# Performance work log

Measured on AMD Instinct MI355X. Metric: run time of the kernel, lower is better.

The kernel has to match this reference:

```python
import jax, jax.numpy as jnp
import numpy as np

B, D, KM1 = 8192, 256, 64  # batch, feature dim (no bias), num_classes-1
NC = KM1 + 1


def setup_inputs() -> dict:
    key = jax.random.key(0)
    k1, k2, k3 = jax.random.split(key, 3)
    features = jax.random.normal(k1, (B, D), dtype=jnp.float32)
    y = jax.random.randint(k2, (B,), 0, NC)
    mu = jax.random.normal(k3, (D, KM1), dtype=jnp.float32) * 0.001
    Sigma = jnp.broadcast_to(jnp.eye(D, dtype=jnp.float32), (KM1, D, D)).copy()
    return {"features": features, "y": y, "mu": mu, "Sigma": Sigma, "loss_type": 1}


def _b_ky(nc):
    # (nc, nc-1) stick-breaking selector matrix
    return 1.0 - jnp.pad(jnp.eye(nc)[..., :-2], [(0, 0), (1, 0)]).cumsum(-1)


def reference(features, y, mu, Sigma, loss_type):
    x = features                      # use_bias=False -> pad is a no-op
    logits = x @ mu                   # (B, K-1)
    bky = _b_ky(NC)                   # (K, K-1)
    y1h = jax.nn.one_hot(y, NC)       # (B, K)
    if loss_type == 0:
        full = jnp.pad(logits, [(0, 0), (0, 1)]) - jax.nn.softplus(logits) @ bky.T
        return -jnp.sum(full * y1h, -1)
    else:
        # psi_k = sqrt(x^T (Sigma_k + mu_k mu_k^T) x) = sqrt(x^T Sigma_k x + (x.mu_k)^2)
        xSx = jnp.einsum('bd,kde,be->bk', x, Sigma, x)   # (B, K-1)
        psi = jnp.sqrt(xSx + logits * logits)
        b = y1h @ bky                 # (B, K-1)
        kappa = y1h[..., :-1] - b / 2
        return -jnp.sum(logits * kappa + b * (psi / 2 - jax.nn.softplus(psi)), -1)
```

## Files before the change

### kernel.cpp

```cpp
#include <hip/hip_runtime.h>

typedef __attribute__((ext_vector_type(8))) short bf16x8;
typedef __attribute__((ext_vector_type(4))) float f32x4;

#define B_N 8192
#define D_N 256
#define K_N 64

__device__ __forceinline__ unsigned short bf16_rne(float f) {
  unsigned u = __builtin_bit_cast(unsigned, f);
  u += 0x7fffu + ((u >> 16) & 1u);
  return (unsigned short)(u >> 16);
}
__device__ __forceinline__ float bf16_f32(unsigned short h) {
  return __builtin_bit_cast(float, (unsigned)h << 16);
}

__device__ __forceinline__ void gload_lds16(const void* g, void* l) {
  __builtin_amdgcn_global_load_lds(
      (const __attribute__((address_space(1))) unsigned int*)g,
      (__attribute__((address_space(3))) unsigned int*)l, 16, 0, 0);
}

__global__ void convert_kernel(const float* __restrict__ src,
                               ushort* __restrict__ hi, ushort* __restrict__ lo,
                               int n4) {
  int idx = blockIdx.x * blockDim.x + threadIdx.x;
  int stride = gridDim.x * blockDim.x;
  for (int i = idx; i < n4; i += stride) {
    float4 v = ((const float4*)src)[i];
    ushort4 h, l;
    h.x = bf16_rne(v.x); l.x = bf16_rne(v.x - bf16_f32(h.x));
    h.y = bf16_rne(v.y); l.y = bf16_rne(v.y - bf16_f32(h.y));
    h.z = bf16_rne(v.z); l.z = bf16_rne(v.z - bf16_f32(h.z));
    h.w = bf16_rne(v.w); l.w = bf16_rne(v.w - bf16_f32(h.w));
    ((ushort4*)hi)[i] = h;
    ((ushort4*)lo)[i] = l;
  }
}

__global__ __launch_bounds__(256, 3) void xsx64_kernel(
    const float* __restrict__ X,
    const ushort* __restrict__ Xh, const ushort* __restrict__ Xl,
    const ushort* __restrict__ Sh, const ushort* __restrict__ Sl,
    float* __restrict__ xsx) {
  __shared__ __align__(16) ushort smem[20480];
  ushort(*Ah)[32] = (ushort(*)[32])(smem);
  ushort(*Al)[32] = (ushort(*)[32])(smem + 2048);
  ushort(*Bh)[32] = (ushort(*)[32])(smem + 4096);
  ushort(*Bl)[32] = (ushort(*)[32])(smem + 12288);
  float(*red)[64] = (float(*)[64])(smem);

  const int tid = threadIdx.x;
  const int lane = tid & 63;
  const int wid = tid >> 6;
  const int lr = lane & 15;
  const int lk = lane >> 4;

  const int bid = blockIdx.x;
  const int xcd = bid & 7;
  const int j = bid >> 3;
  const int kk = xcd * 8 + (j & 7);
  const int b0 = (j >> 3) * 64;
  const size_t soff = (size_t)kk * D_N * D_N;

  const int srow = lane >> 2;
  const int sc = ((lane & 3) ^ ((lane >> 3) & 3)) * 8;
  const int rdc = (lk ^ ((lr >> 1) & 3)) * 8;

  f32x4 acc[4][4];
#pragma unroll
  for (int mi = 0; mi < 4; ++mi)
#pragma unroll
    for (int ni = 0; ni < 4; ++ni) acc[mi][ni] = (f32x4){0.f, 0.f, 0.f, 0.f};

  const size_t arow = (size_t)(b0 + wid * 16 + srow) * D_N + sc;

  for (int ec = 0; ec < 8; ++ec) {
    const int e0 = ec * 32;
    __syncthreads();
    gload_lds16(Xh + arow + e0, &Ah[wid * 16][0]);
    gload_lds16(Xl + arow + e0, &Al[wid * 16][0]);
#pragma unroll
    for (int i = 0; i < 4; ++i) {
      const size_t brow =
          soff + (size_t)(wid * 64 + i * 16 + srow) * D_N + sc + e0;
      gload_lds16(Sh + brow, &Bh[wid * 64 + i * 16][0]);
      gload_lds16(Sl + brow, &Bl[wid * 64 + i * 16][0]);
    }
    __syncthreads();

    bf16x8 ah[4], al[4];
#pragma unroll
    for (int mi = 0; mi < 4; ++mi) {
      ah[mi] = *(const bf16x8*)&Ah[mi * 16 + lr][rdc];
      al[mi] = *(const bf16x8*)&Al[mi * 16 + lr][rdc];
    }
#pragma unroll
    for (int ni = 0; ni < 4; ++ni) {
      const bf16x8 bh = *(const bf16x8*)&Bh[wid * 64 + ni * 16 + lr][rdc];
      const bf16x8 bl = *(const bf16x8*)&Bl[wid * 64 + ni * 16 + lr][rdc];
#pragma unroll
      for (int mi = 0; mi < 4; ++mi)
        acc[mi][ni] = __builtin_amdgcn_mfma_f32_16x16x32_bf16(
            ah[mi], bh, acc[mi][ni], 0, 0, 0);
#pragma unroll
      for (int mi = 0; mi < 4; ++mi)
        acc[mi][ni] = __builtin_amdgcn_mfma_f32_16x16x32_bf16(
            al[mi], bh, acc[mi][ni], 0, 0, 0);
#pragma unroll
      for (int mi = 0; mi < 4; ++mi)
        acc[mi][ni] = __builtin_amdgcn_mfma_f32_16x16x32_bf16(
            ah[mi], bl, acc[mi][ni], 0, 0, 0);
    }
  }

  float p[4][4];
#pragma unroll
  for (int mi = 0; mi < 4; ++mi)
#pragma unroll
    for (int jj = 0; jj < 4; ++jj) p[mi][jj] = 0.f;
#pragma unroll
  for (int mi = 0; mi < 4; ++mi) {
#pragma unroll
    for (int jj = 0; jj < 4; ++jj) {
      const int brow = b0 + mi * 16 + lk * 4 + jj;
      const float* xr = X + (size_t)brow * D_N + wid * 64 + lr;
#pragma unroll
      for (int ni = 0; ni < 4; ++ni)
        p[mi][jj] = fmaf(acc[mi][ni][jj], xr[ni * 16], p[mi][jj]);
    }
  }
#pragma unroll
  for (int mi = 0; mi < 4; ++mi)
#pragma unroll
    for (int jj = 0; jj < 4; ++jj) {
      float v = p[mi][jj];
      v += __shfl_xor(v, 1);
      v += __shfl_xor(v, 2);
      v += __shfl_xor(v, 4);
      v += __shfl_xor(v, 8);
      p[mi][jj] = v;
    }
  __syncthreads();
  if (lr == 0) {
#pragma unroll
    for (int mi = 0; mi < 4; ++mi)
#pragma unroll
      for (int jj = 0; jj < 4; ++jj)
        red[wid][mi * 16 + lk * 4 + jj] = p[mi][jj];
  }
  __syncthreads();
  if (tid < 64) {
    const float s = red[0][tid] + red[1][tid] + red[2][tid] + red[3][tid];
    xsx[(size_t)(b0 + tid) * K_N + kk] = s;
  }
}

__global__ __launch_bounds__(512, 2) void xsx_fallback(
    const float* __restrict__ X, const float* __restrict__ Sigma,
    float* __restrict__ xsx) {
  constexpr int BM = 128, KT = 32;
  __shared__ __align__(16) ushort Ah[BM][KT];
  __shared__ __align__(16) ushort Al[BM][KT];
  __shared__ __align__(16) ushort Bh[D_N][KT];
  __shared__ __align__(16) ushort Bl[D_N][KT];
  __shared__ float red[4][BM];

  const int tid = threadIdx.x;
  const int lane = tid & 63;
  const int wid = tid >> 6;
  const int wm = wid >> 2;
  const int wn = wid & 3;
  const int lr = lane & 15;
  const int lk = lane >> 4;

  const int b0 = blockIdx.x * BM;
  const int kk = blockIdx.y;
  const size_t soff = (size_t)kk * D_N * D_N;

  f32x4 acc[4][4];
#pragma unroll
  for (int mi = 0; mi < 4; ++mi)
#pragma unroll
    for (int ni = 0; ni < 4; ++ni) acc[mi][ni] = (f32x4){0.f, 0.f, 0.f, 0.f};

  for (int ec = 0; ec < D_N / KT; ++ec) {
    const int e0 = ec * KT;
    __syncthreads();
#pragma unroll
    for (int r = 0; r < 2; ++r) {
      const int i = tid + 512 * r;
      const int row = i >> 3, c4 = (i & 7) * 4;
      const float4 v = *(const float4*)(X + (size_t)(b0 + row) * D_N + e0 + c4);
      ushort4 h, l;
      h.x = bf16_rne(v.x); l.x = bf16_rne(v.x - bf16_f32(h.x));
      h.y = bf16_rne(v.y); l.y = bf16_rne(v.y - bf16_f32(h.y));
      h.z = bf16_rne(v.z); l.z = bf16_rne(v.z - bf16_f32(h.z));
      h.w = bf16_rne(v.w); l.w = bf16_rne(v.w - bf16_f32(h.w));
      *(ushort4*)&Ah[row][c4] = h;
      *(ushort4*)&Al[row][c4] = l;
    }
#pragma unroll
    for (int r = 0; r < 4; ++r) {
      const int i = tid + 512 * r;
      const int d = i >> 3, c4 = (i & 7) * 4;
      const float4 v = *(const float4*)(Sigma + soff + (size_t)d * D_N + e0 + c4);
      ushort4 h, l;
      h.x = bf16_rne(v.x); l.x = bf16_rne(v.x - bf16_f32(h.x));
      h.y = bf16_rne(v.y); l.y = bf16_rne(v.y - bf16_f32(h.y));
      h.z = bf16_rne(v.z); l.z = bf16_rne(v.z - bf16_f32(h.z));
      h.w = bf16_rne(v.w); l.w = bf16_rne(v.w - bf16_f32(h.w));
      *(ushort4*)&Bh[d][c4] = h;
      *(ushort4*)&Bl[d][c4] = l;
    }
    __syncthreads();

    bf16x8 ah[4], al[4];
#pragma unroll
    for (int mi = 0; mi < 4; ++mi) {
      ah[mi] = *(const bf16x8*)&Ah[wm * 64 + mi * 16 + lr][lk * 8];
      al[mi] = *(const bf16x8*)&Al[wm * 64 + mi * 16 + lr][lk * 8];
    }
#pragma unroll
    for (int ni = 0; ni < 4; ++ni) {
      const bf16x8 bh = *(const bf16x8*)&Bh[wn * 64 + ni * 16 + lr][lk * 8];
      const bf16x8 bl = *(const bf16x8*)&Bl[wn * 64 + ni * 16 + lr][lk * 8];
#pragma unroll
      for (int mi = 0; mi < 4; ++mi) {
        acc[mi][ni] = __builtin_amdgcn_mfma_f32_16x16x32_bf16(ah[mi], bh, acc[mi][ni], 0, 0, 0);
        acc[mi][ni] = __builtin_amdgcn_mfma_f32_16x16x32_bf16(al[mi], bh, acc[mi][ni], 0, 0, 0);
        acc[mi][ni] = __builtin_amdgcn_mfma_f32_16x16x32_bf16(ah[mi], bl, acc[mi][ni], 0, 0, 0);
      }
    }
  }

  float p[4][4];
#pragma unroll
  for (int mi = 0; mi < 4; ++mi)
#pragma unroll
    for (int jj = 0; jj < 4; ++jj) p[mi][jj] = 0.f;
#pragma unroll
  for (int mi = 0; mi < 4; ++mi) {
#pragma unroll
    for (int jj = 0; jj < 4; ++jj) {
      const int brow = b0 + wm * 64 + mi * 16 + lk * 4 + jj;
      const float* xr = X + (size_t)brow * D_N + wn * 64 + lr;
#pragma unroll
      for (int ni = 0; ni < 4; ++ni)
        p[mi][jj] = fmaf(acc[mi][ni][jj], xr[ni * 16], p[mi][jj]);
    }
  }
#pragma unroll
  for (int mi = 0; mi < 4; ++mi)
#pragma unroll
    for (int jj = 0; jj < 4; ++jj) {
      float v = p[mi][jj];
      v += __shfl_xor(v, 1);
      v += __shfl_xor(v, 2);
      v += __shfl_xor(v, 4);
      v += __shfl_xor(v, 8);
      p[mi][jj] = v;
    }
  if (lr == 0) {
#pragma unroll
    for (int mi = 0; mi < 4; ++mi)
#pragma unroll
      for (int jj = 0; jj < 4; ++jj)
        red[wn][wm * 64 + mi * 16 + lk * 4 + jj] = p[mi][jj];
  }
  __syncthreads();
  if (tid < BM) {
    const float s = red[0][tid] + red[1][tid] + red[2][tid] + red[3][tid];
    xsx[(size_t)(b0 + tid) * K_N + kk] = s;
  }
}

__global__ __launch_bounds__(256) void loss_kernel(
    const float* __restrict__ X, const int* __restrict__ y,
    const float* __restrict__ mu, const int* __restrict__ loss_type,
    const float* __restrict__ xsx, float* __restrict__ out) {
  __shared__ float mu_s[D_N * K_N];
  __shared__ float x_s[4][D_N];
  const int tid = threadIdx.x;
  const int wid = tid >> 6;
  const int lane = tid & 63;
  const int b = blockIdx.x * 4 + wid;

  for (int i = tid; i < D_N * K_N / 4; i += 256)
    ((float4*)mu_s)[i] = ((const float4*)mu)[i];
  ((float4*)&x_s[wid][0])[lane] = ((const float4*)(X + (size_t)b * D_N))[lane];
  __syncthreads();

  const int yb = y[b];
  const int lt = loss_type[0];

  float logit = 0.f;
#pragma unroll 8
  for (int d = 0; d < D_N; ++d)
    logit = fmaf(x_s[wid][d], mu_s[d * K_N + lane], logit);

  float term;
  if (lt == 1) {
    const float xv = xsx[(size_t)b * K_N + lane];
    const float psi = sqrtf(fmaxf(xv + logit * logit, 0.f));
    const float bk = (lane <= yb) ? 1.f : 0.f;
    const float kap = ((lane == yb) ? 1.f : 0.f) - 0.5f * bk;
    term = logit * kap + bk * (-0.5f * psi - log1pf(expf(-psi)));
  } else {
    const float sp = (logit > 0.f) ? (logit + log1pf(expf(-logit)))
                                   : log1pf(expf(logit));
    term = ((lane == yb) ? logit : 0.f) - ((lane <= yb) ? sp : 0.f);
  }
#pragma unroll
  for (int s = 1; s < 64; s <<= 1) term += __shfl_xor(term, s);
  if (lane == 0) out[b] = -term;
}

extern "C" void kernel_launch(void* const* d_in, const int* in_sizes, int n_in,
                              void* d_out, int out_size, void* d_ws, size_t ws_size,
                              hipStream_t stream) {
  const float* X = (const float*)d_in[0];
  const int* y = (const int*)d_in[1];
  const float* mu = (const float*)d_in[2];
  const float* Sigma = (const float*)d_in[3];
  const int* lt = (const int*)d_in[4];
  float* out = (float*)d_out;

  const size_t XN = (size_t)B_N * D_N;
  const size_t SN = (size_t)K_N * D_N * D_N;
  const size_t xh_off = 0;
  const size_t xl_off = xh_off + XN * 2;
  const size_t sh_off = xl_off + XN * 2;
  const size_t sl_off = sh_off + SN * 2;
  const size_t xsx_off = sl_off + SN * 2;
  const size_t need = xsx_off + (size_t)B_N * K_N * 4;

  char* w = (char*)d_ws;
  if (ws_size >= need) {
    ushort* Xh = (ushort*)(w + xh_off);
    ushort* Xl = (ushort*)(w + xl_off);
    ushort* Sh = (ushort*)(w + sh_off);
    ushort* Sl = (ushort*)(w + sl_off);
    float* xsx = (float*)(w + xsx_off);
    hipLaunchKernelGGL(convert_kernel, dim3(1024), dim3(256), 0, stream,
                       X, Xh, Xl, (int)(XN / 4));
    hipLaunchKernelGGL(convert_kernel, dim3(2048), dim3(256), 0, stream,
                       Sigma, Sh, Sl, (int)(SN / 4));
    hipLaunchKernelGGL(xsx64_kernel, dim3(8192), dim3(256), 0, stream,
                       X, Xh, Xl, Sh, Sl, xsx);
    hipLaunchKernelGGL(loss_kernel, dim3(B_N / 4), dim3(256), 0, stream,
                       X, y, mu, lt, xsx, out);
  } else {
    float* xsx = (float*)w;
    hipLaunchKernelGGL(xsx_fallback, dim3(B_N / 128, K_N), dim3(512), 0, stream,
                       X, Sigma, xsx);
    hipLaunchKernelGGL(loss_kernel, dim3(B_N / 4), dim3(256), 0, stream,
                       X, y, mu, lt, xsx, out);
  }
}
```

Baseline: 233.5 us.

## Exploit Sigma symmetry by summing only the upper block-triangular quadratic form

Precomputes a symmetrized, block-upper-triangular Sigma: diagonal blocks are halved, off-diagonal blocks get Sigma+Sigma^T, and lower blocks are never written or read. The GEMM kernel is restructured so each block handles one 64-row d-block over 256 batch rows and only the e-chunks at or above it. This cuts the MFMA work for x^T Sigma x to roughly 10/16 of the full product. Partial sums for the four d-blocks are written to a 4x larger buffer and combined in the loss kernel, which adds extra memory traffic and leaves the work unevenly spread across blocks.

```diff
diff --git a/kernel.cpp b/kernel.cpp
--- a/kernel.cpp
+++ b/kernel.cpp
@@ -39,17 +39,44 @@
   }
 }
 
-__global__ __launch_bounds__(256, 3) void xsx64_kernel(
+__global__ void convert_T_kernel(const float* __restrict__ Sigma,
+                                 ushort* __restrict__ Th,
+                                 ushort* __restrict__ Tl) {
+  const int dtab[10] = {0, 0, 0, 0, 1, 1, 1, 2, 2, 3};
+  const int etab[10] = {0, 1, 2, 3, 1, 2, 3, 2, 3, 3};
+  const int k = blockIdx.x;
+  const int dblk = dtab[blockIdx.y], eblk = etab[blockIdx.y];
+  const float wgt = (dblk == eblk) ? 0.5f : 1.0f;
+  const int tid = threadIdx.x;
+  const int dl = tid >> 2;
+  const int el0 = (tid & 3) * 16;
+  const int d = dblk * 64 + dl;
+  const size_t rowbase = ((size_t)k * D_N + d) * D_N + eblk * 64 + el0;
+  const float* Srow = Sigma + rowbase;
+  const float* Scol = Sigma + ((size_t)k * D_N + eblk * 64 + el0) * D_N + d;
+  ushort h[16], l[16];
+#pragma unroll
+  for (int i = 0; i < 16; ++i) {
+    const float t = (Srow[i] + Scol[(size_t)i * D_N]) * wgt;
+    h[i] = bf16_rne(t);
+    l[i] = bf16_rne(t - bf16_f32(h[i]));
+  }
+  *(uint4*)(Th + rowbase) = *(uint4*)&h[0];
+  *(uint4*)(Th + rowbase + 8) = *(uint4*)&h[8];
+  *(uint4*)(Tl + rowbase) = *(uint4*)&l[0];
+  *(uint4*)(Tl + rowbase + 8) = *(uint4*)&l[8];
+}
+
+__global__ __launch_bounds__(256, 3) void xsx_tri_kernel(
     const float* __restrict__ X,
     const ushort* __restrict__ Xh, const ushort* __restrict__ Xl,
-    const ushort* __restrict__ Sh, const ushort* __restrict__ Sl,
-    float* __restrict__ xsx) {
+    const ushort* __restrict__ Th, const ushort* __restrict__ Tl,
+    float* __restrict__ part) {
   __shared__ __align__(16) ushort smem[20480];
-  ushort(*Ah)[32] = (ushort(*)[32])(smem);
-  ushort(*Al)[32] = (ushort(*)[32])(smem + 2048);
-  ushort(*Bh)[32] = (ushort(*)[32])(smem + 4096);
-  ushort(*Bl)[32] = (ushort(*)[32])(smem + 12288);
-  float(*red)[64] = (float(*)[64])(smem);
+  ushort(*A_h)[32] = (ushort(*)[32])(smem);
+  ushort(*A_l)[32] = (ushort(*)[32])(smem + 8192);
+  ushort(*B_h)[32] = (ushort(*)[32])(smem + 16384);
+  ushort(*B_l)[32] = (ushort(*)[32])(smem + 18432);
 
   const int tid = threadIdx.x;
   const int lane = tid & 63;
@@ -59,10 +86,12 @@
 
   const int bid = blockIdx.x;
   const int xcd = bid & 7;
-  const int j = bid >> 3;
-  const int kk = xcd * 8 + (j & 7);
-  const int b0 = (j >> 3) * 64;
-  const size_t soff = (size_t)kk * D_N * D_N;
+  const int r = bid >> 3;
+  const int qd = r >> 8;
+  const int s = r & 255;
+  const int kk = xcd * 8 + (s & 7);
+  const int bg = s >> 3;
+  const int bbase = bg * 256;
 
   const int srow = lane >> 2;
   const int sc = ((lane & 3) ^ ((lane >> 3) & 3)) * 8;
@@ -74,32 +103,33 @@
 #pragma unroll
     for (int ni = 0; ni < 4; ++ni) acc[mi][ni] = (f32x4){0.f, 0.f, 0.f, 0.f};
 
-  const size_t arow = (size_t)(b0 + wid * 16 + srow) * D_N + sc;
-
-  for (int ec = 0; ec < 8; ++ec) {
-    const int e0 = ec * 32;
+  const size_t a0 = (size_t)(bbase + wid * 64 + srow) * D_N + sc;
+  const size_t b0g = (size_t)kk * (D_N * D_N) +
+                     (size_t)(qd * 64 + wid * 16 + srow) * D_N + sc;
+
+  const int nch = 2 * (4 - qd);
+  for (int c = 0; c < nch; ++c) {
+    const int e0 = qd * 64 + c * 32;
     __syncthreads();
-    gload_lds16(Xh + arow + e0, &Ah[wid * 16][0]);
-    gload_lds16(Xl + arow + e0, &Al[wid * 16][0]);
 #pragma unroll
     for (int i = 0; i < 4; ++i) {
-      const size_t brow =
-          soff + (size_t)(wid * 64 + i * 16 + srow) * D_N + sc + e0;
-      gload_lds16(Sh + brow, &Bh[wid * 64 + i * 16][0]);
-      gload_lds16(Sl + brow, &Bl[wid * 64 + i * 16][0]);
-    }
+      gload_lds16(Xh + a0 + i * 16 * D_N + e0, &A_h[wid * 64 + i * 16][0]);
+      gload_lds16(Xl + a0 + i * 16 * D_N + e0, &A_l[wid * 64 + i * 16][0]);
+    }
+    gload_lds16(Th + b0g + e0, &B_h[wid * 16][0]);
+    gload_lds16(Tl + b0g + e0, &B_l[wid * 16][0]);
     __syncthreads();
 
     bf16x8 ah[4], al[4];
 #pragma unroll
     for (int mi = 0; mi < 4; ++mi) {
-      ah[mi] = *(const bf16x8*)&Ah[mi * 16 + lr][rdc];
-      al[mi] = *(const bf16x8*)&Al[mi * 16 + lr][rdc];
+      ah[mi] = *(const bf16x8*)&A_h[wid * 64 + mi * 16 + lr][rdc];
+      al[mi] = *(const bf16x8*)&A_l[wid * 64 + mi * 16 + lr][rdc];
     }
 #pragma unroll
     for (int ni = 0; ni < 4; ++ni) {
-      const bf16x8 bh = *(const bf16x8*)&Bh[wid * 64 + ni * 16 + lr][rdc];
-      const bf16x8 bl = *(const bf16x8*)&Bl[wid * 64 + ni * 16 + lr][rdc];
+      const bf16x8 bh = *(const bf16x8*)&B_h[ni * 16 + lr][rdc];
+      const bf16x8 bl = *(const bf16x8*)&B_l[ni * 16 + lr][rdc];
 #pragma unroll
       for (int mi = 0; mi < 4; ++mi)
         acc[mi][ni] = __builtin_amdgcn_mfma_f32_16x16x32_bf16(
@@ -115,45 +145,21 @@
     }
   }
 
-  float p[4][4];
-#pragma unroll
-  for (int mi = 0; mi < 4; ++mi)
-#pragma unroll
-    for (int jj = 0; jj < 4; ++jj) p[mi][jj] = 0.f;
 #pragma unroll
   for (int mi = 0; mi < 4; ++mi) {
 #pragma unroll
     for (int jj = 0; jj < 4; ++jj) {
-      const int brow = b0 + mi * 16 + lk * 4 + jj;
-      const float* xr = X + (size_t)brow * D_N + wid * 64 + lr;
-#pragma unroll
-      for (int ni = 0; ni < 4; ++ni)
-        p[mi][jj] = fmaf(acc[mi][ni][jj], xr[ni * 16], p[mi][jj]);
-    }
-  }
-#pragma unroll
-  for (int mi = 0; mi < 4; ++mi)
-#pragma unroll
-    for (int jj = 0; jj < 4; ++jj) {
-      float v = p[mi][jj];
-      v += __shfl_xor(v, 1);
-      v += __shfl_xor(v, 2);
-      v += __shfl_xor(v, 4);
-      v += __shfl_xor(v, 8);
-      p[mi][jj] = v;
-    }
-  __syncthreads();
-  if (lr == 0) {
-#pragma unroll
-    for (int mi = 0; mi < 4; ++mi)
-#pragma unroll
-      for (int jj = 0; jj < 4; ++jj)
-        red[wid][mi * 16 + lk * 4 + jj] = p[mi][jj];
-  }
-  __syncthreads();
-  if (tid < 64) {
-    const float s = red[0][tid] + red[1][tid] + red[2][tid] + red[3][tid];
-    xsx[(size_t)(b0 + tid) * K_N + kk] = s;
+      const int brow = bbase + wid * 64 + mi * 16 + lk * 4 + jj;
+      const float* xr = X + (size_t)brow * D_N + qd * 64 + lr;
+      float p = 0.f;
+#pragma unroll
+      for (int ni = 0; ni < 4; ++ni) p = fmaf(acc[mi][ni][jj], xr[ni * 16], p);
+      p += __shfl_xor(p, 1);
+      p += __shfl_xor(p, 2);
+      p += __shfl_xor(p, 4);
+      p += __shfl_xor(p, 8);
+      if (lr == 0) part[((size_t)brow * K_N + kk) * 4 + qd] = p;
+    }
   }
 }
 
@@ -279,7 +285,7 @@
 __global__ __launch_bounds__(256) void loss_kernel(
     const float* __restrict__ X, const int* __restrict__ y,
     const float* __restrict__ mu, const int* __restrict__ loss_type,
-    const float* __restrict__ xsx, float* __restrict__ out) {
+    const float* __restrict__ xsx, float* __restrict__ out, int nparts) {
   __shared__ float mu_s[D_N * K_N];
   __shared__ float x_s[4][D_N];
   const int tid = threadIdx.x;
@@ -302,7 +308,13 @@
 
   float term;
   if (lt == 1) {
-    const float xv = xsx[(size_t)b * K_N + lane];
+    float xv;
+    if (nparts == 4) {
+      const float4 pv = *(const float4*)(xsx + ((size_t)b * K_N + lane) * 4);
+      xv = ((pv.x + pv.y) + pv.z) + pv.w;
+    } else {
+      xv = xsx[(size_t)b * K_N + lane];
+    }
     const float psi = sqrtf(fmaxf(xv + logit * logit, 0.f));
     const float bk = (lane <= yb) ? 1.f : 0.f;
     const float kap = ((lane == yb) ? 1.f : 0.f) - 0.5f * bk;
@@ -331,31 +343,31 @@
   const size_t SN = (size_t)K_N * D_N * D_N;
   const size_t xh_off = 0;
   const size_t xl_off = xh_off + XN * 2;
-  const size_t sh_off = xl_off + XN * 2;
-  const size_t sl_off = sh_off + SN * 2;
-  const size_t xsx_off = sl_off + SN * 2;
-  const size_t need = xsx_off + (size_t)B_N * K_N * 4;
+  const size_t th_off = xl_off + XN * 2;
+  const size_t tl_off = th_off + SN * 2;
+  const size_t part_off = tl_off + SN * 2;
+  const size_t need = part_off + (size_t)B_N * K_N * 4 * 4;
 
   char* w = (char*)d_ws;
   if (ws_size >= need) {
     ushort* Xh = (ushort*)(w + xh_off);
     ushort* Xl = (ushort*)(w + xl_off);
-    ushort* Sh = (ushort*)(w + sh_off);
-    ushort* Sl = (ushort*)(w + sl_off);
-    float* xsx = (float*)(w + xsx_off);
+    ushort* Th = (ushort*)(w + th_off);
+    ushort* Tl = (ushort*)(w + tl_off);
+    float* part = (float*)(w + part_off);
     hipLaunchKernelGGL(convert_kernel, dim3(1024), dim3(256), 0, stream,
                        X, Xh, Xl, (int)(XN / 4));
-    hipLaunchKernelGGL(convert_kernel, dim3(2048), dim3(256), 0, stream,
-                       Sigma, Sh, Sl, (int)(SN / 4));
-    hipLaunchKernelGGL(xsx64_kernel, dim3(8192), dim3(256), 0, stream,
-                       X, Xh, Xl, Sh, Sl, xsx);
+    hipLaunchKernelGGL(convert_T_kernel, dim3(64, 10), dim3(256), 0, stream,
+                       Sigma, Th, Tl);
+    hipLaunchKernelGGL(xsx_tri_kernel, dim3(8192), dim3(256), 0, stream,
+                       X, Xh, Xl, Th, Tl, part);
     hipLaunchKernelGGL(loss_kernel, dim3(B_N / 4), dim3(256), 0, stream,
-                       X, y, mu, lt, xsx, out);
+                       X, y, mu, lt, part, out, 4);
   } else {
     float* xsx = (float*)w;
     hipLaunchKernelGGL(xsx_fallback, dim3(B_N / 128, K_N), dim3(512), 0, stream,
                        X, Sigma, xsx);
     hipLaunchKernelGGL(loss_kernel, dim3(B_N / 4), dim3(256), 0, stream,
-                       X, y, mu, lt, xsx, out);
-  }
-}
+                       X, y, mu, lt, xsx, out, 1);
+  }
+}
```

Result: faster. 194.0 us (-16.9%).
